# Performance work log

Measured on AMD Instinct MI355X. Metric: run time of the kernel, lower is better.

## Reference

```python
import jax, jax.numpy as jnp
import numpy as np

# dims (match init_kwargs / input_specs)
B, T, D = 64, 512, 128
H = 256          # hidden_size
W = 32           # cell_size
N = 64           # n_slots
R = 4            # n_reads
L = 2            # ctl_n_layers
TAU = 0.3
CLIP = 20.0
RW = R * W                      # read_size = 128
CTL_IN = D + RW                 # 256
CTL_OUT = 2 * RW + W + W        # 2*read + write cell + erase = 320
EPS = 1e-8


def setup_inputs() -> dict:
    key = jax.random.key(0)
    ks = jax.random.split(key, 10)
    s = lambda k, shape: jax.random.normal(k, shape, jnp.float32) * 0.05
    return {
        "x": jax.random.normal(ks[0], (B, T, D), jnp.float32),
        "h0": jax.random.normal(ks[1], (L, B, H), jnp.float32) * 0.1,
        # GRU layer 0 (PyTorch layout: [3H, in])
        "W_ih0": s(ks[2], (3 * H, CTL_IN)), "W_hh0": s(ks[3], (3 * H, H)),
        "b_ih0": jnp.zeros((3 * H,), jnp.float32), "b_hh0": jnp.zeros((3 * H,), jnp.float32),
        # GRU layer 1
        "W_ih1": s(ks[4], (3 * H, H)), "W_hh1": s(ks[5], (3 * H, H)),
        "b_ih1": jnp.zeros((3 * H,), jnp.float32), "b_hh1": jnp.zeros((3 * H,), jnp.float32),
        # interface Linear(H -> CTL_OUT) + ReLU
        "W_int": s(ks[6], (CTL_OUT, H)), "b_int": jnp.zeros((CTL_OUT,), jnp.float32),
        # mix gate Linear(2W -> W)
        "W_mix": s(ks[7], (W, 2 * W)), "b_mix": jnp.zeros((W,), jnp.float32),
    }


def _gru(xt, h, Wih, Whh, bih, bhh):
    gi = xt @ Wih.T + bih
    gh = h @ Whh.T + bhh
    ir, iz, inn = jnp.split(gi, 3, axis=-1)
    hr, hz, hn = jnp.split(gh, 3, axis=-1)
    r = jax.nn.sigmoid(ir + hr)
    z = jax.nn.sigmoid(iz + hz)
    n = jnp.tanh(inn + r * hn)
    return (1.0 - z) * n + z * h


def _cos_read(k, M, tau):
    # k: [b,R,W] keys, M: [b,N,W] memory -> content-based softmax read
    kn = k / (jnp.linalg.norm(k, axis=-1, keepdims=True) + EPS)
    Mn = M / (jnp.linalg.norm(M, axis=-1, keepdims=True) + EPS)
    w = jax.nn.softmax(jnp.einsum('brw,bnw->brn', kn, Mn) / tau, axis=-1)
    return jnp.einsum('brn,bnw->brw', w, M), w


def _forward(x, h0, W_ih0, W_hh0, b_ih0, b_hh0, W_ih1, W_hh1, b_ih1, b_hh1,
             W_int, b_int, W_mix, b_mix):
    bs = x.shape[0]

    def step(carry, inp):
        h0c, h1c, em, bm, l_read = carry
        xt, t = inp
        ctl = jnp.concatenate([xt, l_read], axis=-1)
        h0n = _gru(ctl, h0c, W_ih0, W_hh0, b_ih0, b_hh0)
        h1n = _gru(h0n, h1c, W_ih1, W_hh1, b_ih1, b_hh1)
        itf = jnp.clip(jax.nn.relu(h1n @ W_int.T + b_int), -CLIP, CLIP)
        k_em = itf[:, :RW].reshape(bs, R, W)
        k_bm = itf[:, RW:2 * RW].reshape(bs, R, W)
        m_t = itf[:, 2 * RW:2 * RW + W]          # write vector
        e_t = itf[:, 2 * RW + W:]                # erase vector
        # explicit memory: round-robin slot write (slot = t mod N), erase old content
        oh = jax.nn.one_hot(t % N, N, dtype=em.dtype)            # [N]
        em_erased = jnp.einsum('n,bnw->bw', oh, em)              # evicted slot
        em_new = em * (1.0 - oh)[None, :, None] + oh[None, :, None] * m_t[:, None, :]
        em_read, _ = _cos_read(k_em, em_new, TAU)
        # blurred memory: content read, then erase/accumulate evicted explicit slot
        bm_read, wb = _cos_read(k_bm, bm, 1.0)
        ww = wb.mean(axis=1)                                     # [b,N] write weights
        e = jax.nn.sigmoid(e_t)                                  # [b,W] bounded erase
        bm_new = bm * (1.0 - ww[:, :, None] * e[:, None, :]) \
                 + ww[:, :, None] * em_erased[:, None, :]
        # mix gate between explicit and blurred reads (per read head)
        g = jax.nn.sigmoid(jnp.concatenate([em_read, bm_read], -1) @ W_mix.T + b_mix)
        read = g * em_read + (1.0 - g) * bm_read                 # [b,R,W]
        l_new = read.reshape(bs, RW)
        out_t = jnp.concatenate([h0n, h1n, l_new], axis=-1)      # [b, 2H+RW]
        return (h0n, h1n, em_new, bm_new, l_new), out_t

    em0 = jnp.zeros((bs, N, W), x.dtype)
    bm0 = jnp.zeros((bs, N, W), x.dtype)
    lr0 = jnp.zeros((bs, RW), x.dtype)
    carry0 = (h0[0], h0[1], em0, bm0, lr0)
    xs = (jnp.swapaxes(x, 0, 1), jnp.arange(x.shape[1]))
    _, outs = jax.lax.scan(step, carry0, xs)                     # [T,b,2H+RW]
    return jnp.swapaxes(outs, 0, 1)                              # [b,T,2H+RW]


def reference(x, h0, W_ih0, W_hh0, b_ih0, b_hh0, W_ih1, W_hh1, b_ih1, b_hh1,
              W_int, b_int, W_mix, b_mix):
    return _forward(x, h0, W_ih0, W_hh0, b_ih0, b_hh0, W_ih1, W_hh1, b_ih1,
                    b_hh1, W_int, b_int, W_mix, b_mix)
```

## Files before the change

kernel.cpp:

```cpp
#include <hip/hip_runtime.h>
#include <hip/hip_bf16.h>
#include <hip/hip_fp16.h>
#include <stdint.h>

typedef unsigned int uint;
typedef unsigned short ushort;

#define TPB 768

#define OFF_A0 0
#define OFF_A1 (768*256)
#define OFF_A2 (2*768*256)
#define OFF_A3 (3*768*256)
#define OFF_A4 (4*768*256)
#define WS_USHORTS (4*768*256 + 320*256)

__device__ __forceinline__ __half2 h2cast(uint u){
    union { uint u; __half2 h; } c; c.u = u; return c.h;
}
__device__ __forceinline__ float sigm(float x){ return 1.0f / (1.0f + __expf(-x)); }
__device__ __forceinline__ float tanh_(float x){
    float xc = fminf(fmaxf(x, -15.0f), 15.0f);
    float e  = __expf(2.0f * xc);
    return (e - 1.0f) / (e + 1.0f);
}

__global__ void prep_kernel(const float* __restrict__ Wih0, const float* __restrict__ Whh0,
                            const float* __restrict__ Wih1, const float* __restrict__ Whh1,
                            const float* __restrict__ Wint, ushort* __restrict__ ws)
{
    int idx = blockIdx.x * 256 + threadIdx.x;
    if (idx >= WS_USHORTS) return;
    const float* src; int rows; int base; int p;
    if (idx < 4*768*256) {
        int m = idx / (768*256); p = idx % (768*256);
        src  = (m==0) ? Wih0 : (m==1) ? Whh0 : (m==2) ? Wih1 : Whh1;
        rows = 768; base = m * (768*256);
    } else {
        p = idx - 4*768*256; src = Wint; rows = 320; base = 4*768*256;
    }
    int kb  = p / (rows*8);
    int rem = p - kb*(rows*8);
    int j   = rem >> 3;
    int kl  = rem & 7;
    int k   = kb*8 + kl;
    __half h = __float2half_rn(src[j*256 + k]);
    ws[base + p] = *reinterpret_cast<ushort*>(&h);
}

template<int ROWS>
__device__ __forceinline__ void mv2_row(const ushort* __restrict__ W, const float* vin,
                                        float b0, float b1, float* o0, float* o1,
                                        int j0, int j1)
{
    const uint4* P = (const uint4*)W;
    float p0a = b0, p0b = 0.f, p1a = b1, p1b = 0.f;
#pragma unroll 4
    for (int kb = 0; kb < 32; ++kb) {
        uint4 w0 = P[kb*ROWS + j0];
        uint4 w1 = P[kb*ROWS + j1];
        float4 va = *(const float4*)&vin[kb*8];
        float4 vb = *(const float4*)&vin[kb*8 + 4];
        __half2 h;
        h = h2cast(w0.x); p0a += __low2float(h)*va.x; p0a += __high2float(h)*va.y;
        h = h2cast(w0.y); p0a += __low2float(h)*va.z; p0a += __high2float(h)*va.w;
        h = h2cast(w0.z); p0b += __low2float(h)*vb.x; p0b += __high2float(h)*vb.y;
        h = h2cast(w0.w); p0b += __low2float(h)*vb.z; p0b += __high2float(h)*vb.w;
        h = h2cast(w1.x); p1a += __low2float(h)*va.x; p1a += __high2float(h)*va.y;
        h = h2cast(w1.y); p1a += __low2float(h)*va.z; p1a += __high2float(h)*va.w;
        h = h2cast(w1.z); p1b += __low2float(h)*vb.x; p1b += __high2float(h)*vb.y;
        h = h2cast(w1.w); p1b += __low2float(h)*vb.z; p1b += __high2float(h)*vb.w;
    }
    *o0 = p0a + p0b;
    *o1 = p1a + p1b;
}

__global__ __launch_bounds__(TPB) void ebm_main(
    const float* __restrict__ x, const float* __restrict__ h0i,
    const float* __restrict__ b_ih0, const float* __restrict__ b_hh0,
    const float* __restrict__ b_ih1, const float* __restrict__ b_hh1,
    const float* __restrict__ b_int, const float* __restrict__ Wmix,
    const float* __restrict__ bmix,
    const ushort* __restrict__ ws, float* __restrict__ out)
{
    __shared__ float v[256];
    __shared__ float gi[768], gh[768];
    __shared__ float h0s[256], h1s[256];
    __shared__ float lread[128];
    __shared__ float em[64][33], bm[64][33];
    __shared__ float itf[320];
    __shared__ float minv_em[64], minv_bm[64], kinv[8];
    __shared__ float sc[8][64];
    __shared__ float wwv[64], ev[32], emer[32];
    __shared__ float emrd[4][32], bmrd[4][32];
    __shared__ float wmix_s[32][65];

    const int tid = threadIdx.x;
    const int b   = blockIdx.x;

    if (tid < 256) { h0s[tid] = h0i[b*256 + tid]; h1s[tid] = h0i[(64 + b)*256 + tid]; }
    for (int i = tid; i < 64*33; i += TPB) { (&em[0][0])[i] = 0.f; (&bm[0][0])[i] = 0.f; }
    if (tid < 128) lread[tid] = 0.f;
    for (int i = tid; i < 32*64; i += TPB) { wmix_s[i >> 6][i & 63] = Wmix[i]; }
    __syncthreads();

    for (int t = 0; t < 512; ++t) {
        const size_t outbase = ((size_t)b*512 + t) * 640;

        if (tid < 128)      v[tid] = x[((size_t)b*512 + t)*128 + tid];
        else if (tid < 256) v[tid] = lread[tid - 128];
        __syncthreads();

        if (tid < 384) {
            mv2_row<768>(ws + OFF_A0, v, b_ih0[tid], b_ih0[tid + 384],
                         &gi[tid], &gi[tid + 384], tid, tid + 384);
        } else {
            int i = tid - 384;
            mv2_row<768>(ws + OFF_A1, h0s, b_hh0[i], b_hh0[i + 384],
                         &gh[i], &gh[i + 384], i, i + 384);
        }
        __syncthreads();
        if (tid < 256) {
            float r  = sigm(gi[tid]       + gh[tid]);
            float z  = sigm(gi[256 + tid] + gh[256 + tid]);
            float n  = tanh_(gi[512 + tid] + r * gh[512 + tid]);
            float hn = (1.f - z) * n + z * h0s[tid];
            h0s[tid] = hn;
            out[outbase + tid] = hn;
        }
        __syncthreads();

        if (tid < 384) {
            mv2_row<768>(ws + OFF_A2, h0s, b_ih1[tid], b_ih1[tid + 384],
                         &gi[tid], &gi[tid + 384], tid, tid + 384);
        } else {
            int i = tid - 384;
            mv2_row<768>(ws + OFF_A3, h1s, b_hh1[i], b_hh1[i + 384],
                         &gh[i], &gh[i + 384], i, i + 384);
        }
        __syncthreads();
        if (tid < 256) {
            float r  = sigm(gi[tid]       + gh[tid]);
            float z  = sigm(gi[256 + tid] + gh[256 + tid]);
            float n  = tanh_(gi[512 + tid] + r * gh[512 + tid]);
            float hn = (1.f - z) * n + z * h1s[tid];
            h1s[tid] = hn;
            out[outbase + 256 + tid] = hn;
        }
        __syncthreads();

        if (tid < 160) {
            float a0, a1;
            mv2_row<320>(ws + OFF_A4, h1s, b_int[tid], b_int[tid + 160],
                         &a0, &a1, tid, tid + 160);
            itf[tid]       = fminf(fmaxf(a0, 0.f), 20.f);
            itf[tid + 160] = fminf(fmaxf(a1, 0.f), 20.f);
        }
        __syncthreads();

        const int slot = t & 63;
        if (tid < 32) {
            emer[tid] = em[slot][tid];
            em[slot][tid] = itf[256 + tid];
            ev[tid] = sigm(itf[288 + tid]);
        }
        if (tid >= 32 && tid < 40) {
            int r = tid - 32;
            const float* kk = &itf[r*32];
            float s = 0.f;
#pragma unroll
            for (int w2 = 0; w2 < 32; ++w2) { float q = kk[w2]; s += q*q; }
            kinv[r] = 1.f / (sqrtf(s) + 1e-8f);
        }
        __syncthreads();

        if (tid < 64) {
            float s = 0.f;
#pragma unroll
            for (int w2 = 0; w2 < 32; ++w2) { float q = em[tid][w2]; s += q*q; }
            minv_em[tid] = 1.f / (sqrtf(s) + 1e-8f);
        } else if (tid < 128) {
            int n = tid - 64; float s = 0.f;
#pragma unroll
            for (int w2 = 0; w2 < 32; ++w2) { float q = bm[n][w2]; s += q*q; }
            minv_bm[n] = 1.f / (sqrtf(s) + 1e-8f);
        }
        __syncthreads();

        if (tid < 512) {
            int mm = tid >> 8, r = (tid >> 6) & 3, n = tid & 63;
            const float* kk = &itf[mm*128 + r*32];
            const float (*M)[33] = mm ? bm : em;
            float d = 0.f;
#pragma unroll
            for (int w2 = 0; w2 < 32; ++w2) d += kk[w2] * M[n][w2];
            float val = d * kinv[mm*4 + r] * (mm ? minv_bm[n] : minv_em[n]);
            if (!mm) val *= (1.f/0.3f);
            sc[mm*4 + r][n] = val;
        }
        __syncthreads();

        {
            int wave = tid >> 6, lane = tid & 63;
            if (wave < 8) {
                float val = sc[wave][lane];
                float m = val;
                for (int o = 32; o > 0; o >>= 1) m = fmaxf(m, __shfl_xor(m, o));
                float e = __expf(val - m);
                float s = e;
                for (int o = 32; o > 0; o >>= 1) s += __shfl_xor(s, o);
                sc[wave][lane] = e / s;
            }
        }
        __syncthreads();

        if (tid < 64) wwv[tid] = 0.25f * (sc[4][tid] + sc[5][tid] + sc[6][tid] + sc[7][tid]);
        if (tid < 256) {
            int mm = tid >> 7, r = (tid >> 5) & 3, w2 = tid & 31;
            const float (*M)[33] = mm ? bm : em;
            const float* wr = sc[mm*4 + r];
            float a = 0.f;
#pragma unroll 8
            for (int n = 0; n < 64; ++n) a += wr[n] * M[n][w2];
            if (mm) bmrd[r][w2] = a; else emrd[r][w2] = a;
        }
        __syncthreads();

        if (tid < 128) {
            int r = tid >> 5, w2 = tid & 31;
            float a = bmix[w2];
#pragma unroll
            for (int c = 0; c < 32; ++c) a += wmix_s[w2][c]      * emrd[r][c];
#pragma unroll
            for (int c = 0; c < 32; ++c) a += wmix_s[w2][32 + c] * bmrd[r][c];
            float g  = sigm(a);
            float rd = g * emrd[r][w2] + (1.f - g) * bmrd[r][w2];
            lread[tid] = rd;
            out[outbase + 512 + tid] = rd;
        } else {
            for (int i2 = tid - 128; i2 < 2048; i2 += TPB - 128) {
                int n = i2 >> 5, w2 = i2 & 31;
                bm[n][w2] = bm[n][w2] * (1.f - wwv[n]*ev[w2]) + wwv[n]*emer[w2];
            }
        }
        __syncthreads();
    }
}

extern "C" void kernel_launch(void* const* d_in, const int* in_sizes, int n_in,
                              void* d_out, int out_size, void* d_ws, size_t ws_size,
                              hipStream_t stream)
{
    const float* x    = (const float*)d_in[0];
    const float* h0   = (const float*)d_in[1];
    const float* Wih0 = (const float*)d_in[2];
    const float* Whh0 = (const float*)d_in[3];
    const float* bih0 = (const float*)d_in[4];
    const float* bhh0 = (const float*)d_in[5];
    const float* Wih1 = (const float*)d_in[6];
    const float* Whh1 = (const float*)d_in[7];
    const float* bih1 = (const float*)d_in[8];
    const float* bhh1 = (const float*)d_in[9];
    const float* Wint = (const float*)d_in[10];
    const float* bint = (const float*)d_in[11];
    const float* Wmix = (const float*)d_in[12];
    const float* bmix = (const float*)d_in[13];
    ushort* ws = (ushort*)d_ws;
    float*  out = (float*)d_out;

    if (ws_size < (size_t)WS_USHORTS * sizeof(ushort)) return;

    prep_kernel<<<(WS_USHORTS + 255)/256, 256, 0, stream>>>(Wih0, Whh0, Wih1, Whh1, Wint, ws);
    ebm_main<<<64, TPB, 0, stream>>>(x, h0, bih0, bhh0, bih1, bhh1, bint, Wmix, bmix, ws, out);
}
```

Before: 12.47 ms.

## Precompute x-projection of layer-0 GRU input and software-pipeline weight loads

Adds a parallel pre-kernel that computes the x part of the layer-0 input projection (plus bias) for all timesteps into workspace. The recurrent kernel then only multiplies the read vector half of W_ih0 each step, taking that work off the serial critical path. The matvec helper now double-buffers weight loads across chunks of four k-blocks, which raises register use. Memory-norm computation is also merged into the interface stage to remove one barrier, with the freshly written slot's norm recomputed inline. The fast path needs a large extra workspace buffer and falls back to the old path if the workspace is too small.

Measured after the change: 30.99 ms. 2.48x slower.

```diff
diff --git a/kernel.cpp b/kernel.cpp
--- a/kernel.cpp
+++ b/kernel.cpp
@@ -14,6 +14,8 @@
 #define OFF_A3 (3*768*256)
 #define OFF_A4 (4*768*256)
 #define WS_USHORTS (4*768*256 + 320*256)
+#define WB_BYTES ((size_t)WS_USHORTS * 2)
+#define GIXP_FLOATS ((size_t)64*512*768)
 
 __device__ __forceinline__ __half2 h2cast(uint u){
     union { uint u; __half2 h; } c; c.u = u; return c.h;
@@ -48,31 +50,97 @@
     ws[base + p] = *reinterpret_cast<ushort*>(&h);
 }
 
-template<int ROWS>
-__device__ __forceinline__ void mv2_row(const ushort* __restrict__ W, const float* vin,
-                                        float b0, float b1, float* o0, float* o1,
-                                        int j0, int j1)
+__global__ __launch_bounds__(256) void xp_kernel(const float* __restrict__ x,
+        const float* __restrict__ bih0, const ushort* __restrict__ ws,
+        float* __restrict__ gixp)
+{
+    __shared__ float xs[32][132];
+    __shared__ float ys[32][129];
+    const int tid = threadIdx.x;
+    const int b   = blockIdx.x >> 4;
+    const int t0  = (blockIdx.x & 15) * 32;
+    for (int i = tid; i < 32*32; i += 256) {
+        int t = i >> 5, kq = i & 31;
+        *(float4*)&xs[t][kq*4] = *(const float4*)&x[((size_t)(b*512 + t0 + t))*128 + kq*4];
+    }
+    __syncthreads();
+    const int rg = tid >> 5;
+    const int t  = tid & 31;
+    float xr[128];
+#pragma unroll
+    for (int kq = 0; kq < 32; ++kq) {
+        float4 f = *(const float4*)&xs[t][kq*4];
+        xr[kq*4+0]=f.x; xr[kq*4+1]=f.y; xr[kq*4+2]=f.z; xr[kq*4+3]=f.w;
+    }
+    const uint4* P = (const uint4*)ws;
+#pragma unroll 1
+    for (int rc = 0; rc < 6; ++rc) {
+        __syncthreads();
+#pragma unroll 1
+        for (int s = 0; s < 16; ++s) {
+            int j = rg*96 + rc*16 + s;
+            float pa = bih0[j], pb = 0.f;
+#pragma unroll
+            for (int kb = 0; kb < 16; ++kb) {
+                uint4 w = P[kb*768 + j];
+                __half2 h;
+                h=h2cast(w.x); pa += __low2float(h)*xr[kb*8+0]; pa += __high2float(h)*xr[kb*8+1];
+                h=h2cast(w.y); pa += __low2float(h)*xr[kb*8+2]; pa += __high2float(h)*xr[kb*8+3];
+                h=h2cast(w.z); pb += __low2float(h)*xr[kb*8+4]; pb += __high2float(h)*xr[kb*8+5];
+                h=h2cast(w.w); pb += __low2float(h)*xr[kb*8+6]; pb += __high2float(h)*xr[kb*8+7];
+            }
+            ys[t][rg*16 + s] = pa + pb;
+        }
+        __syncthreads();
+        for (int i2 = tid; i2 < 32*128; i2 += 256) {
+            int t2 = i2 >> 7, c = i2 & 127;
+            int j  = (c >> 4)*96 + rc*16 + (c & 15);
+            gixp[((size_t)(b*512 + t0 + t2))*768 + j] = ys[t2][c];
+        }
+    }
+}
+
+#define FMA8(W0, W1, KB) { \
+    float4 va = *(const float4*)&vin[(KB)*8]; \
+    float4 vb = *(const float4*)&vin[(KB)*8 + 4]; \
+    __half2 h; \
+    h=h2cast((W0).x); p0 += __low2float(h)*va.x; p0 += __high2float(h)*va.y; \
+    h=h2cast((W0).y); p0 += __low2float(h)*va.z; p0 += __high2float(h)*va.w; \
+    h=h2cast((W0).z); q0 += __low2float(h)*vb.x; q0 += __high2float(h)*vb.y; \
+    h=h2cast((W0).w); q0 += __low2float(h)*vb.z; q0 += __high2float(h)*vb.w; \
+    h=h2cast((W1).x); p1 += __low2float(h)*va.x; p1 += __high2float(h)*va.y; \
+    h=h2cast((W1).y); p1 += __low2float(h)*va.z; p1 += __high2float(h)*va.w; \
+    h=h2cast((W1).z); q1 += __low2float(h)*vb.x; q1 += __high2float(h)*vb.y; \
+    h=h2cast((W1).w); q1 += __low2float(h)*vb.z; q1 += __high2float(h)*vb.w; }
+
+template<int ROWS, int NKB>
+__device__ __forceinline__ void mv2_pipe(const ushort* __restrict__ W, const float* vin,
+                                         float b0, float b1, float* o0, float* o1,
+                                         int j0, int j1)
 {
     const uint4* P = (const uint4*)W;
-    float p0a = b0, p0b = 0.f, p1a = b1, p1b = 0.f;
-#pragma unroll 4
-    for (int kb = 0; kb < 32; ++kb) {
-        uint4 w0 = P[kb*ROWS + j0];
-        uint4 w1 = P[kb*ROWS + j1];
-        float4 va = *(const float4*)&vin[kb*8];
-        float4 vb = *(const float4*)&vin[kb*8 + 4];
-        __half2 h;
-        h = h2cast(w0.x); p0a += __low2float(h)*va.x; p0a += __high2float(h)*va.y;
-        h = h2cast(w0.y); p0a += __low2float(h)*va.z; p0a += __high2float(h)*va.w;
-        h = h2cast(w0.z); p0b += __low2float(h)*vb.x; p0b += __high2float(h)*vb.y;
-        h = h2cast(w0.w); p0b += __low2float(h)*vb.z; p0b += __high2float(h)*vb.w;
-        h = h2cast(w1.x); p1a += __low2float(h)*va.x; p1a += __high2float(h)*va.y;
-        h = h2cast(w1.y); p1a += __low2float(h)*va.z; p1a += __high2float(h)*va.w;
-        h = h2cast(w1.z); p1b += __low2float(h)*vb.x; p1b += __high2float(h)*vb.y;
-        h = h2cast(w1.w); p1b += __low2float(h)*vb.z; p1b += __high2float(h)*vb.w;
-    }
-    *o0 = p0a + p0b;
-    *o1 = p1a + p1b;
+    float p0 = b0, q0 = 0.f, p1 = b1, q1 = 0.f;
+    uint4 c0[4], c1[4];
+#pragma unroll
+    for (int u = 0; u < 4; ++u) { c0[u] = P[u*ROWS + j0]; c1[u] = P[u*ROWS + j1]; }
+#pragma unroll
+    for (int ch = 0; ch < NKB/4; ++ch) {
+        uint4 n0[4], n1[4];
+        if (ch + 1 < NKB/4) {
+#pragma unroll
+            for (int u = 0; u < 4; ++u) {
+                n0[u] = P[((ch+1)*4 + u)*ROWS + j0];
+                n1[u] = P[((ch+1)*4 + u)*ROWS + j1];
+            }
+        }
+#pragma unroll
+        for (int u = 0; u < 4; ++u) { FMA8(c0[u], c1[u], ch*4 + u); }
+        if (ch + 1 < NKB/4) {
+#pragma unroll
+            for (int u = 0; u < 4; ++u) { c0[u] = n0[u]; c1[u] = n1[u]; }
+        }
+    }
+    *o0 = p0 + q0; *o1 = p1 + q1;
 }
 
 __global__ __launch_bounds__(TPB) void ebm_main(
@@ -81,7 +149,8 @@
     const float* __restrict__ b_ih1, const float* __restrict__ b_hh1,
     const float* __restrict__ b_int, const float* __restrict__ Wmix,
     const float* __restrict__ bmix,
-    const ushort* __restrict__ ws, float* __restrict__ out)
+    const ushort* __restrict__ ws, const float* __restrict__ gixp, int use_xp,
+    float* __restrict__ out)
 {
     __shared__ float v[256];
     __shared__ float gi[768], gh[768];
@@ -107,17 +176,28 @@
     for (int t = 0; t < 512; ++t) {
         const size_t outbase = ((size_t)b*512 + t) * 640;
 
-        if (tid < 128)      v[tid] = x[((size_t)b*512 + t)*128 + tid];
-        else if (tid < 256) v[tid] = lread[tid - 128];
+        if (use_xp) {
+            gi[tid] = gixp[((size_t)(b*512 + t))*768 + tid];
+            if (tid < 128) v[tid] = lread[tid];
+        } else {
+            if (tid < 128)      v[tid] = x[((size_t)b*512 + t)*128 + tid];
+            else if (tid < 256) v[tid] = lread[tid - 128];
+        }
         __syncthreads();
 
         if (tid < 384) {
-            mv2_row<768>(ws + OFF_A0, v, b_ih0[tid], b_ih0[tid + 384],
-                         &gi[tid], &gi[tid + 384], tid, tid + 384);
+            if (use_xp) {
+                float bb0 = gi[tid], bb1 = gi[tid + 384];
+                mv2_pipe<768,16>(ws + OFF_A0 + 16*768*8, v, bb0, bb1,
+                                 &gi[tid], &gi[tid + 384], tid, tid + 384);
+            } else {
+                mv2_pipe<768,32>(ws + OFF_A0, v, b_ih0[tid], b_ih0[tid + 384],
+                                 &gi[tid], &gi[tid + 384], tid, tid + 384);
+            }
         } else {
             int i = tid - 384;
-            mv2_row<768>(ws + OFF_A1, h0s, b_hh0[i], b_hh0[i + 384],
-                         &gh[i], &gh[i + 384], i, i + 384);
+            mv2_pipe<768,32>(ws + OFF_A1, h0s, b_hh0[i], b_hh0[i + 384],
+                             &gh[i], &gh[i + 384], i, i + 384);
         }
         __syncthreads();
         if (tid < 256) {
@@ -131,12 +211,12 @@
         __syncthreads();
 
         if (tid < 384) {
-            mv2_row<768>(ws + OFF_A2, h0s, b_ih1[tid], b_ih1[tid + 384],
-                         &gi[tid], &gi[tid + 384], tid, tid + 384);
+            mv2_pipe<768,32>(ws + OFF_A2, h0s, b_ih1[tid], b_ih1[tid + 384],
+                             &gi[tid], &gi[tid + 384], tid, tid + 384);
         } else {
             int i = tid - 384;
-            mv2_row<768>(ws + OFF_A3, h1s, b_hh1[i], b_hh1[i + 384],
-                         &gh[i], &gh[i + 384], i, i + 384);
+            mv2_pipe<768,32>(ws + OFF_A3, h1s, b_hh1[i], b_hh1[i + 384],
+                             &gh[i], &gh[i + 384], i, i + 384);
         }
         __syncthreads();
         if (tid < 256) {
@@ -149,41 +229,37 @@
         }
         __syncthreads();
 
+        const int slot = t & 63;
         if (tid < 160) {
             float a0, a1;
-            mv2_row<320>(ws + OFF_A4, h1s, b_int[tid], b_int[tid + 160],
-                         &a0, &a1, tid, tid + 160);
+            mv2_pipe<320,32>(ws + OFF_A4, h1s, b_int[tid], b_int[tid + 160],
+                             &a0, &a1, tid, tid + 160);
             itf[tid]       = fminf(fmaxf(a0, 0.f), 20.f);
             itf[tid + 160] = fminf(fmaxf(a1, 0.f), 20.f);
-        }
-        __syncthreads();
-
-        const int slot = t & 63;
+        } else if (tid >= 320 && tid < 384) {
+            int n = tid - 320; float s = 0.f;
+#pragma unroll
+            for (int w2 = 0; w2 < 32; ++w2) { float q = em[n][w2]; s += q*q; }
+            minv_em[n] = 1.f / (sqrtf(s) + 1e-8f);
+        } else if (tid >= 384 && tid < 448) {
+            int n = tid - 384; float s = 0.f;
+#pragma unroll
+            for (int w2 = 0; w2 < 32; ++w2) { float q = bm[n][w2]; s += q*q; }
+            minv_bm[n] = 1.f / (sqrtf(s) + 1e-8f);
+        }
+        __syncthreads();
+
         if (tid < 32) {
             emer[tid] = em[slot][tid];
             em[slot][tid] = itf[256 + tid];
             ev[tid] = sigm(itf[288 + tid]);
-        }
-        if (tid >= 32 && tid < 40) {
+        } else if (tid < 40) {
             int r = tid - 32;
             const float* kk = &itf[r*32];
             float s = 0.f;
 #pragma unroll
             for (int w2 = 0; w2 < 32; ++w2) { float q = kk[w2]; s += q*q; }
             kinv[r] = 1.f / (sqrtf(s) + 1e-8f);
-        }
-        __syncthreads();
-
-        if (tid < 64) {
-            float s = 0.f;
-#pragma unroll
-            for (int w2 = 0; w2 < 32; ++w2) { float q = em[tid][w2]; s += q*q; }
-            minv_em[tid] = 1.f / (sqrtf(s) + 1e-8f);
-        } else if (tid < 128) {
-            int n = tid - 64; float s = 0.f;
-#pragma unroll
-            for (int w2 = 0; w2 < 32; ++w2) { float q = bm[n][w2]; s += q*q; }
-            minv_bm[n] = 1.f / (sqrtf(s) + 1e-8f);
         }
         __syncthreads();
 
@@ -191,10 +267,12 @@
             int mm = tid >> 8, r = (tid >> 6) & 3, n = tid & 63;
             const float* kk = &itf[mm*128 + r*32];
             const float (*M)[33] = mm ? bm : em;
-            float d = 0.f;
-#pragma unroll
-            for (int w2 = 0; w2 < 32; ++w2) d += kk[w2] * M[n][w2];
-            float val = d * kinv[mm*4 + r] * (mm ? minv_bm[n] : minv_em[n]);
+            float d = 0.f, ss = 0.f;
+#pragma unroll
+            for (int w2 = 0; w2 < 32; ++w2) { float m_ = M[n][w2]; d += kk[w2]*m_; ss += m_*m_; }
+            float minv = mm ? minv_bm[n]
+                            : ((n == slot) ? 1.f/(sqrtf(ss) + 1e-8f) : minv_em[n]);
+            float val = d * kinv[mm*4 + r] * minv;
             if (!mm) val *= (1.f/0.3f);
             sc[mm*4 + r][n] = val;
         }
@@ -265,11 +343,17 @@
     const float* bint = (const float*)d_in[11];
     const float* Wmix = (const float*)d_in[12];
     const float* bmix = (const float*)d_in[13];
-    ushort* ws = (ushort*)d_ws;
+    ushort* ws  = (ushort*)d_ws;
     float*  out = (float*)d_out;
 
-    if (ws_size < (size_t)WS_USHORTS * sizeof(ushort)) return;
+    if (ws_size < WB_BYTES) return;
+    const size_t need_xp = WB_BYTES + GIXP_FLOATS * 4;
+    const int use_xp = (ws_size >= need_xp) ? 1 : 0;
+    float* gixp = (float*)((char*)d_ws + WB_BYTES);
 
     prep_kernel<<<(WS_USHORTS + 255)/256, 256, 0, stream>>>(Wih0, Whh0, Wih1, Whh1, Wint, ws);
-    ebm_main<<<64, TPB, 0, stream>>>(x, h0, bih0, bhh0, bih1, bhh1, bint, Wmix, bmix, ws, out);
-}
+    if (use_xp)
+        xp_kernel<<<64*16, 256, 0, stream>>>(x, bih0, ws, gixp);
+    ebm_main<<<64, TPB, 0, stream>>>(x, h0, bih0, bhh0, bih1, bhh1, bint, Wmix, bmix,
+                                     ws, gixp, use_xp, out);
+}
```
